# Performance work log

Hardware: AMD Instinct MI355X
Metric: run time of the kernel (lower is better)

The kernel has to match this reference:

```python
import jax, jax.numpy as jnp
import numpy as np
import math

B, S, D, H = 2, 2048, 1024, 16
DK = D // H
NUM_BUCKETS = 32
MAX_DISTANCE = 128


def _relative_position_bucket(relative_position, num_buckets=NUM_BUCKETS, max_distance=MAX_DISTANCE):
    # Bidirectional bucketing, faithful to the torch implementation.
    nb = num_buckets // 2
    n = -relative_position
    ret = (n < 0).astype(jnp.int32) * nb
    n = jnp.abs(n)
    max_exact = nb // 2
    is_small = n < max_exact
    # guard log(0); is_small branch covers n < max_exact anyway
    val_if_large = max_exact + (
        jnp.log(jnp.maximum(n, 1).astype(jnp.float32) / max_exact)
        / math.log(max_distance / max_exact)
        * (nb - max_exact)
    ).astype(jnp.int32)
    val_if_large = jnp.minimum(val_if_large, nb - 1)
    return ret + jnp.where(is_small, n, val_if_large)


def setup_inputs() -> dict:
    key = jax.random.key(0)
    ks = jax.random.split(key, 6)
    scale = 1.0 / math.sqrt(D)
    return {
        "hidden_states": jax.random.normal(ks[0], (B, S, D), dtype=jnp.float32),
        "Wq": jax.random.normal(ks[1], (D, D), dtype=jnp.float32) * scale,
        "Wk": jax.random.normal(ks[2], (D, D), dtype=jnp.float32) * scale,
        "Wv": jax.random.normal(ks[3], (D, D), dtype=jnp.float32) * scale,
        "Wo": jax.random.normal(ks[4], (D, D), dtype=jnp.float32) * scale,
        "rel_emb": jax.random.normal(ks[5], (NUM_BUCKETS, H), dtype=jnp.float32) * 0.1,
    }


def reference(hidden_states, Wq, Wk, Wv, Wo, rel_emb):
    b, s, d = hidden_states.shape
    # nn.Linear convention: y = x @ W.T
    q = jnp.einsum("bsd,ed->bse", hidden_states, Wq).reshape(b, s, H, DK).transpose(0, 2, 1, 3)
    k = jnp.einsum("bsd,ed->bse", hidden_states, Wk).reshape(b, s, H, DK).transpose(0, 2, 1, 3)
    v = jnp.einsum("bsd,ed->bse", hidden_states, Wv).reshape(b, s, H, DK).transpose(0, 2, 1, 3)
    scores = jnp.einsum("bhqd,bhkd->bhqk", q, k) / math.sqrt(DK)  # [B,H,S,S]
    # T5 relative position bias
    ctx = jnp.arange(s)[:, None]
    mem = jnp.arange(s)[None, :]
    rp_bucket = _relative_position_bucket(mem - ctx)          # [S,S]
    bias = rel_emb[rp_bucket]                                  # [S,S,H]
    bias = bias.transpose(2, 0, 1)[None]                       # [1,H,S,S]
    scores = scores + bias
    attn = jax.nn.softmax(scores, axis=-1)
    out = jnp.einsum("bhqk,bhkd->bhqd", attn, v)               # [B,H,S,DK]
    out = out.transpose(0, 2, 1, 3).reshape(b, s, d)
    return jnp.einsum("bsd,ed->bse", out, Wo)
```

## Files before the change

kernel.cpp:

```cpp
#include <hip/hip_runtime.h>
#include <hip/hip_bf16.h>
#include <cstdint>
#include <cstddef>

typedef __bf16 bf16;
typedef __attribute__((ext_vector_type(8))) __bf16 bf16x8;
typedef __attribute__((ext_vector_type(4))) __bf16 bf16x4;
typedef __attribute__((ext_vector_type(4))) float f32x4;
typedef __attribute__((ext_vector_type(4))) short s16x4;

#define B_ 2
#define S_ 2048
#define D_ 1024
#define H_ 16
#define DK_ 64
#define NROWS (B_*S_)
#define NBIAS 4095
#define LDQ 3072
#define LOG2E 1.44269504f

__device__ __forceinline__ void async16(void* lds, const void* g) {
  __builtin_amdgcn_global_load_lds(
      (const __attribute__((address_space(1))) void*)g,
      (__attribute__((address_space(3))) void*)lds, 16, 0, 0);
}

__device__ __forceinline__ f32x4 mfma16(bf16x8 a, bf16x8 b, f32x4 c) {
  return __builtin_amdgcn_mfma_f32_16x16x32_bf16(a, b, c, 0, 0, 0);
}

__device__ __forceinline__ s16x4 bc4(bf16x4 x) {
  union { bf16x4 b; s16x4 s; } u; u.b = x; return u.s;
}

__device__ __forceinline__ f32x4 mfma16k(bf16x4 a, bf16x4 b, f32x4 c) {
  return __builtin_amdgcn_mfma_f32_16x16x16bf16_1k(bc4(a), bc4(b), c, 0, 0, 0);
}

__device__ __forceinline__ float exp2_hw(float x) {
  return __builtin_amdgcn_exp2f(x);
}

__global__ void prep_kernel(const float* __restrict__ X,
                            const float* __restrict__ Wq, const float* __restrict__ Wk,
                            const float* __restrict__ Wv, const float* __restrict__ Wo,
                            const float* __restrict__ rel_emb,
                            bf16* __restrict__ Xb, bf16* __restrict__ oqkv,
                            bf16* __restrict__ oo, float* __restrict__ tab) {
  const int bid = blockIdx.x;
  const int tid = threadIdx.x;
  if (bid < 4096) {
    int i = bid * 256 + tid;
    float4 v = ((const float4*)X)[i];
    bf16x4 o;
    o[0] = (bf16)v.x; o[1] = (bf16)v.y; o[2] = (bf16)v.z; o[3] = (bf16)v.w;
    ((bf16x4*)Xb)[i] = o;
  } else if (bid < 8192) {
    int widx = bid - 4096;
    int y = widx >> 10;
    const float* src = (y == 0) ? Wq : (y == 1) ? Wk : (y == 2) ? Wv : Wo;
    bf16* dst = (y < 3) ? (oqkv + (size_t)y * D_ * D_) : oo;
    int i = (widx & 1023) * 256 + tid;
    float4 v = ((const float4*)src)[i];
    bf16x4 o;
    o[0] = (bf16)v.x; o[1] = (bf16)v.y; o[2] = (bf16)v.z; o[3] = (bf16)v.w;
    ((bf16x4*)dst)[i] = o;
  } else {
    int idx = (bid - 8192) * 256 + tid;
    if (idx >= H_ * NBIAS) return;
    int h = idx / NBIAS;
    int p = idx - h * NBIAS;
    int rel = p - 2047;
    int n = -rel;
    int ret = 0;
    if (n < 0) { ret = 16; n = -n; }
    int bucket;
    if (n < 8) {
      bucket = ret + n;
    } else {
      double v = log((double)n / 8.0) / log(16.0) * 8.0;
      int vi = 8 + (int)v;
      if (vi > 15) vi = 15;
      bucket = ret + vi;
    }
    tab[idx] = rel_emb[bucket * H_ + h] * LOG2E;
  }
}

template<int OUT_BF16, int MF, int VT_EP>
__global__ __launch_bounds__(256, 3)
void gemm_bt(const bf16* __restrict__ A, const bf16* __restrict__ Bw,
             void* __restrict__ C, bf16* __restrict__ VT, int vThr,
             int M, int N, int K, int colThr, float a0, float a1) {
  __shared__ bf16 smem[MF * 32 * 64 + 128 * 64];
  bf16* As = smem;
  bf16* Bs = smem + MF * 32 * 64;
  const int tid = threadIdx.x;
  const int lane = tid & 63;
  const int w = tid >> 6;
  const int wr = w >> 1, wc = w & 1;
  const int l15 = lane & 15, lhi = lane >> 4;
  const int m0 = blockIdx.y * (MF * 32), n0 = blockIdx.x * 128;
  const float alpha = (n0 < colThr) ? a0 : a1;

  f32x4 acc[MF][4] = {};

  const int urow = tid >> 3;
  const int uswz = (tid & 7) ^ (urow & 7);
  const bf16* ga = A  + (size_t)(m0 + urow) * K + uswz * 8;
  const bf16* gb = Bw + (size_t)(n0 + urow) * K + uswz * 8;

  for (int kt = 0; kt < K; kt += 64) {
#pragma unroll
    for (int rnd = 0; rnd < MF; ++rnd)
      async16(As + tid * 8 + rnd * 2048, ga + kt + (size_t)(rnd * 32) * K);
#pragma unroll
    for (int rnd = 0; rnd < 4; ++rnd)
      async16(Bs + tid * 8 + rnd * 2048, gb + kt + (size_t)(rnd * 32) * K);
    __syncthreads();

#pragma unroll
    for (int kc = 0; kc < 2; ++kc) {
      bf16x8 af[MF], bfr[4];
#pragma unroll
      for (int m = 0; m < MF; ++m) {
        int row = wr * (MF * 16) + m * 16 + l15;
        int off = (row * 64 + kc * 32 + lhi * 8) ^ ((row & 7) << 3);
        af[m] = *(const bf16x8*)&As[off];
      }
#pragma unroll
      for (int n = 0; n < 4; ++n) {
        int row = wc * 64 + n * 16 + l15;
        int off = (row * 64 + kc * 32 + lhi * 8) ^ ((row & 7) << 3);
        bfr[n] = *(const bf16x8*)&Bs[off];
      }
      __builtin_amdgcn_s_setprio(1);
#pragma unroll
      for (int m = 0; m < MF; ++m)
#pragma unroll
        for (int n = 0; n < 4; ++n)
          acc[m][n] = mfma16(af[m], bfr[n], acc[m][n]);
      __builtin_amdgcn_s_setprio(0);
    }
    __syncthreads();
  }

  if (VT_EP && n0 >= vThr) {
    bf16* T = smem;
#pragma unroll
    for (int m = 0; m < MF; ++m)
#pragma unroll
      for (int n = 0; n < 4; ++n)
#pragma unroll
        for (int r = 0; r < 4; ++r) {
          int rl = wr * (MF * 16) + m * 16 + lhi * 4 + r;
          int cl = wc * 64 + n * 16 + l15;
          T[cl * 128 + (rl ^ ((cl & 7) << 3))] = (bf16)(acc[m][n][r] * alpha);
        }
    __syncthreads();
    const int bb = m0 >> 11, s0l = m0 & 2047, d0 = n0 - vThr;
    const int dr = tid >> 1, sh = tid & 1;
    bf16* dst = VT + ((size_t)(bb * 1024 + d0 + dr)) * 2048 + s0l + sh * 64;
    const bf16* src = T + dr * 128;
#pragma unroll
    for (int i = 0; i < 8; ++i) {
      int sb = sh * 8 + i;
      *(bf16x8*)(dst + i * 8) = *(const bf16x8*)(src + ((sb ^ (dr & 7)) * 8));
    }
    return;
  }

#pragma unroll
  for (int m = 0; m < MF; ++m)
#pragma unroll
    for (int n = 0; n < 4; ++n)
#pragma unroll
      for (int r = 0; r < 4; ++r) {
        int row = m0 + wr * (MF * 16) + m * 16 + lhi * 4 + r;
        int col = n0 + wc * 64 + n * 16 + l15;
        float v = acc[m][n][r] * alpha;
        if (OUT_BF16) ((bf16*)C)[(size_t)row * N + col] = (bf16)v;
        else          ((float*)C)[(size_t)row * N + col] = v;
      }
}

__global__ __launch_bounds__(256, 4)
void attn_fwd(const bf16* __restrict__ QKV, const bf16* __restrict__ VTg_,
              const float* __restrict__ biasTab, const float* __restrict__ rel_emb,
              bf16* __restrict__ Og) {
  __shared__ bf16 Ks[2][64 * 64];
  __shared__ bf16 VTs[2][64 * 64];
  __shared__ float bias_s[512];
  const int tid = threadIdx.x;
  const int lane = tid & 63, w = tid >> 6;
  const int l15 = lane & 15, lhi = lane >> 4;
  const int wg = blockIdx.x;
  const int bh = wg & 31, qt = wg >> 5;
  const int b = bh >> 4, h = bh & 15;
  const int q0 = qt * 64;

  for (int i = tid; i < 512; i += 256)
    bias_s[i] = biasTab[h * NBIAS + 1791 + i];

  const float cL = rel_emb[15 * H_ + h] * LOG2E;
  const float cR = rel_emb[31 * H_ + h] * LOG2E;

  bf16x8 qa[2];
  {
    const bf16* Qbase = QKV + (size_t)(b * S_ + q0 + w * 16) * LDQ + h * DK_;
#pragma unroll
    for (int c = 0; c < 2; ++c)
      qa[c] = *(const bf16x8*)(Qbase + (size_t)l15 * LDQ + c * 32 + lhi * 8);
  }

  int koff[8];
#pragma unroll
  for (int kf = 0; kf < 4; ++kf)
#pragma unroll
    for (int c = 0; c < 2; ++c) {
      int krow = kf * 16 + l15;
      koff[kf * 2 + c] = ((krow * 64 + c * 32 + lhi * 8) ^ ((krow & 7) << 3)) * 2;
    }
  int voff[16];
#pragma unroll
  for (int df = 0; df < 4; ++df)
#pragma unroll
    for (int kf = 0; kf < 4; ++kf)
      voff[df * 4 + kf] =
          (((df * 16 + l15) * 64 + kf * 16 + lhi * 4) * 2) ^ ((l15 & 7) << 4);

  float lpart = 0.f;
  f32x4 oacc[4] = {};

  const int urow = tid >> 3;
  const int uswz = (tid & 7) ^ (urow & 7);
  const bf16* gk = QKV  + (size_t)(b * S_) * LDQ + 1024 + h * DK_
                        + (size_t)urow * LDQ + uswz * 8;
  const bf16* gv = VTg_ + (size_t)(b * 1024 + h * DK_) * 2048
                        + (size_t)urow * 2048 + uswz * 8;

  async16(&Ks[0][tid * 8],         gk);
  async16(&Ks[0][tid * 8 + 2048],  gk + 32 * LDQ);
  async16(&VTs[0][tid * 8],        gv);
  async16(&VTs[0][tid * 8 + 2048], gv + 32 * 2048);
  gk += 64 * LDQ;
  gv += 64;
  __syncthreads();

#define TILE_BODY(CUR, KT, DO_PF)                                              \
  do {                                                                         \
    if (DO_PF) {                                                               \
      async16(&Ks[(CUR) ^ 1][tid * 8],         gk);                            \
      async16(&Ks[(CUR) ^ 1][tid * 8 + 2048],  gk + 32 * LDQ);                 \
      async16(&VTs[(CUR) ^ 1][tid * 8],        gv);                            \
      async16(&VTs[(CUR) ^ 1][tid * 8 + 2048], gv + 32 * 2048);                \
      gk += 64 * LDQ;                                                          \
      gv += 64;                                                                \
    }                                                                          \
    const int dk0 = (KT) - q0;                                                 \
    f32x4 st[4];                                                               \
    if (dk0 >= -128 && dk0 <= 128) {                                           \
      const int bb0 = dk0 + lhi * 4 - (w * 16 + l15) + 256;                    \
      _Pragma("unroll")                                                        \
      for (int kf = 0; kf < 4; ++kf)                                           \
        _Pragma("unroll")                                                      \
        for (int r = 0; r < 4; ++r)                                            \
          st[kf][r] = bias_s[bb0 + kf * 16 + r];                               \
    } else {                                                                   \
      const float cq = (dk0 > 0) ? cR : cL;                                    \
      _Pragma("unroll")                                                        \
      for (int kf = 0; kf < 4; ++kf)                                           \
        _Pragma("unroll")                                                      \
        for (int r = 0; r < 4; ++r)                                            \
          st[kf][r] = cq;                                                      \
    }                                                                          \
    _Pragma("unroll")                                                          \
    for (int kf = 0; kf < 4; ++kf) {                                           \
      _Pragma("unroll")                                                        \
      for (int c = 0; c < 2; ++c) {                                            \
        bf16x8 kb = *(const bf16x8*)((const char*)&Ks[CUR][0] +                \
                                     koff[kf * 2 + c]);                        \
        st[kf] = mfma16(kb, qa[c], st[kf]);                                    \
      }                                                                        \
    }                                                                          \
    bf16x4 pa[4];                                                              \
    float rs = 0.f;                                                            \
    _Pragma("unroll")                                                          \
    for (int kf = 0; kf < 4; ++kf)                                             \
      _Pragma("unroll")                                                        \
      for (int r = 0; r < 4; ++r) {                                            \
        float p = exp2_hw(st[kf][r]);                                          \
        rs += p;                                                               \
        pa[kf][r] = (bf16)p;                                                   \
      }                                                                        \
    lpart += rs;                                                               \
    _Pragma("unroll")                                                          \
    for (int df = 0; df < 4; ++df) {                                           \
      bf16x4 vb[4];                                                            \
      _Pragma("unroll")                                                        \
      for (int kf = 0; kf < 4; ++kf)                                           \
        vb[kf] = *(const bf16x4*)((const char*)&VTs[CUR][0] +                  \
                                  voff[df * 4 + kf]);                          \
      _Pragma("unroll")                                                        \
      for (int kf = 0; kf < 4; ++kf)                                           \
        oacc[df] = mfma16k(pa[kf], vb[kf], oacc[df]);                          \
    }                                                                          \
    __syncthreads();                                                           \
  } while (0)

  for (int tt = 0; tt < 16; ++tt) {
    const int ktbase = tt * 128;
    TILE_BODY(0, ktbase, true);
    TILE_BODY(1, ktbase + 64, tt < 15);
  }
#undef TILE_BODY

  float lr0 = lpart;
  lr0 += __shfl_xor(lr0, 16);
  lr0 += __shfl_xor(lr0, 32);
#pragma unroll
  for (int r = 0; r < 4; ++r) {
    float lr = __shfl(lr0, lhi * 4 + r);
    float inv = 1.0f / lr;
#pragma unroll
    for (int df = 0; df < 4; ++df) {
      int row = b * S_ + q0 + w * 16 + lhi * 4 + r;
      int col = h * DK_ + df * 16 + l15;
      Og[(size_t)row * D_ + col] = (bf16)(oacc[df][r] * inv);
    }
  }
}

extern "C" void kernel_launch(void* const* d_in, const int* in_sizes, int n_in,
                              void* d_out, int out_size, void* d_ws, size_t ws_size,
                              hipStream_t stream) {
  const float* X   = (const float*)d_in[0];
  const float* Wq  = (const float*)d_in[1];
  const float* Wk  = (const float*)d_in[2];
  const float* Wv  = (const float*)d_in[3];
  const float* Wo  = (const float*)d_in[4];
  const float* rel = (const float*)d_in[5];
  float* out = (float*)d_out;
  char* ws = (char*)d_ws;
  const size_t MB = 1u << 20;
  bf16* Xb    = (bf16*)(ws + 0 * MB);
  bf16* Wqkvb = (bf16*)(ws + 8 * MB);
  bf16* Wob   = (bf16*)(ws + 14 * MB);
  bf16* QKVb  = (bf16*)(ws + 16 * MB);
  bf16* VTb   = (bf16*)(ws + 40 * MB);
  float* biasTab = (float*)(ws + 48 * MB);

  prep_kernel<<<8448, 256, 0, stream>>>(X, Wq, Wk, Wv, Wo, rel,
                                        Xb, Wqkvb, Wob, biasTab);

  gemm_bt<1, 4, 1><<<dim3(24, 32), 256, 0, stream>>>(Xb, Wqkvb, QKVb,
      VTb, 2048,
      NROWS, 3 * D_, D_, 1024, 0.125f * LOG2E, 1.0f);

  attn_fwd<<<1024, 256, 0, stream>>>(QKVb, VTb, biasTab, rel, Xb );

  gemm_bt<0, 2, 0><<<dim3(8, 64), 256, 0, stream>>>(Xb, Wob, out,
      nullptr, 1 << 30,
      NROWS, D_, D_, 0, 1.0f, 1.0f);
}
```

Measured before the change: 114.9 us.

## Process two query fragments per wave to double K/V tile reuse in attention

Each attention workgroup now covers 128 query rows instead of 64, with each wave holding two 16-row Q fragments, so every K and V^T tile loaded into LDS feeds twice as many MFMAs. The grid halves to 512 blocks and launch bounds drop to 2 waves per SIMD to leave room for the doubled accumulators. The bias window indexing is adjusted for the wider query span. The aim is to halve K/V global and LDS traffic per unit of work, at the cost of fewer blocks (fewer than two per CU on 256 CUs) and lower occupancy.

```diff
diff --git a/kernel.cpp b/kernel.cpp
--- a/kernel.cpp
+++ b/kernel.cpp
@@ -184,7 +184,7 @@
       }
 }
 
-__global__ __launch_bounds__(256, 4)
+__global__ __launch_bounds__(256, 2)
 void attn_fwd(const bf16* __restrict__ QKV, const bf16* __restrict__ VTg_,
               const float* __restrict__ biasTab, const float* __restrict__ rel_emb,
               bf16* __restrict__ Og) {
@@ -197,20 +197,22 @@
   const int wg = blockIdx.x;
   const int bh = wg & 31, qt = wg >> 5;
   const int b = bh >> 4, h = bh & 15;
-  const int q0 = qt * 64;
-
-  for (int i = tid; i < 512; i += 256)
-    bias_s[i] = biasTab[h * NBIAS + 1791 + i];
+  const int q0 = qt * 128;
+
+  for (int i = tid; i < 511; i += 256)
+    bias_s[i] = biasTab[h * NBIAS + 1792 + i];
 
   const float cL = rel_emb[15 * H_ + h] * LOG2E;
   const float cR = rel_emb[31 * H_ + h] * LOG2E;
 
-  bf16x8 qa[2];
+  bf16x8 qa[2][2];
   {
-    const bf16* Qbase = QKV + (size_t)(b * S_ + q0 + w * 16) * LDQ + h * DK_;
-#pragma unroll
-    for (int c = 0; c < 2; ++c)
-      qa[c] = *(const bf16x8*)(Qbase + (size_t)l15 * LDQ + c * 32 + lhi * 8);
+    const bf16* Qbase = QKV + (size_t)(b * S_ + q0 + w * 32) * LDQ + h * DK_;
+#pragma unroll
+    for (int qf = 0; qf < 2; ++qf)
+#pragma unroll
+      for (int c = 0; c < 2; ++c)
+        qa[qf][c] = *(const bf16x8*)(Qbase + (size_t)(qf * 16 + l15) * LDQ + c * 32 + lhi * 8);
   }
 
   int koff[8];
@@ -229,8 +231,8 @@
       voff[df * 4 + kf] =
           (((df * 16 + l15) * 64 + kf * 16 + lhi * 4) * 2) ^ ((l15 & 7) << 4);
 
-  float lpart = 0.f;
-  f32x4 oacc[4] = {};
+  float lpart[2] = {0.f, 0.f};
+  f32x4 oacc[2][4] = {};
 
   const int urow = tid >> 3;
   const int uswz = (tid & 7) ^ (urow & 7);
@@ -258,21 +260,25 @@
       gv += 64;                                                                \
     }                                                                          \
     const int dk0 = (KT) - q0;                                                 \
-    f32x4 st[4];                                                               \
-    if (dk0 >= -128 && dk0 <= 128) {                                           \
-      const int bb0 = dk0 + lhi * 4 - (w * 16 + l15) + 256;                    \
-      _Pragma("unroll")                                                        \
-      for (int kf = 0; kf < 4; ++kf)                                           \
+    f32x4 st[2][4];                                                            \
+    if (dk0 >= -128 && dk0 <= 192) {                                           \
+      const int bb0 = dk0 + lhi * 4 - w * 32 - l15 + 255;                      \
+      _Pragma("unroll")                                                        \
+      for (int qf = 0; qf < 2; ++qf)                                           \
         _Pragma("unroll")                                                      \
-        for (int r = 0; r < 4; ++r)                                            \
-          st[kf][r] = bias_s[bb0 + kf * 16 + r];                               \
+        for (int kf = 0; kf < 4; ++kf)                                         \
+          _Pragma("unroll")                                                    \
+          for (int r = 0; r < 4; ++r)                                          \
+            st[qf][kf][r] = bias_s[bb0 + (kf - qf) * 16 + r];                  \
     } else {                                                                   \
       const float cq = (dk0 > 0) ? cR : cL;                                    \
       _Pragma("unroll")                                                        \
-      for (int kf = 0; kf < 4; ++kf)                                           \
+      for (int qf = 0; qf < 2; ++qf)                                           \
         _Pragma("unroll")                                                      \
-        for (int r = 0; r < 4; ++r)                                            \
-          st[kf][r] = cq;                                                      \
+        for (int kf = 0; kf < 4; ++kf)                                         \
+          _Pragma("unroll")                                                    \
+          for (int r = 0; r < 4; ++r)                                          \
+            st[qf][kf][r] = cq;                                                \
     }                                                                          \
     _Pragma("unroll")                                                          \
     for (int kf = 0; kf < 4; ++kf) {                                           \
@@ -280,20 +286,24 @@
       for (int c = 0; c < 2; ++c) {                                            \
         bf16x8 kb = *(const bf16x8*)((const char*)&Ks[CUR][0] +                \
                                      koff[kf * 2 + c]);                        \
-        st[kf] = mfma16(kb, qa[c], st[kf]);                                    \
+        st[0][kf] = mfma16(kb, qa[0][c], st[0][kf]);                           \
+        st[1][kf] = mfma16(kb, qa[1][c], st[1][kf]);                           \
       }                                                                        \
     }                                                                          \
-    bf16x4 pa[4];                                                              \
-    float rs = 0.f;                                                            \
+    bf16x4 pa[2][4];                                                           \
     _Pragma("unroll")                                                          \
-    for (int kf = 0; kf < 4; ++kf)                                             \
-      _Pragma("unroll")                                                        \
-      for (int r = 0; r < 4; ++r) {                                            \
-        float p = exp2_hw(st[kf][r]);                                          \
-        rs += p;                                                               \
-        pa[kf][r] = (bf16)p;                                                   \
-      }                                                                        \
-    lpart += rs;                                                               \
+    for (int qf = 0; qf < 2; ++qf) {                                           \
+      float rs = 0.f;                                                          \
+      _Pragma("unroll")                                                        \
+      for (int kf = 0; kf < 4; ++kf)                                           \
+        _Pragma("unroll")                                                      \
+        for (int r = 0; r < 4; ++r) {                                          \
+          float p = exp2_hw(st[qf][kf][r]);                                    \
+          rs += p;                                                             \
+          pa[qf][kf][r] = (bf16)p;                                             \
+        }                                                                      \
+      lpart[qf] += rs;                                                         \
+    }                                                                          \
     _Pragma("unroll")                                                          \
     for (int df = 0; df < 4; ++df) {                                           \
       bf16x4 vb[4];                                                            \
@@ -302,8 +312,10 @@
         vb[kf] = *(const bf16x4*)((const char*)&VTs[CUR][0] +                  \
                                   voff[df * 4 + kf]);                          \
       _Pragma("unroll")                                                        \
-      for (int kf = 0; kf < 4; ++kf)                                           \
-        oacc[df] = mfma16k(pa[kf], vb[kf], oacc[df]);                          \
+      for (int qf = 0; qf < 2; ++qf)                                           \
+        _Pragma("unroll")                                                      \
+        for (int kf = 0; kf < 4; ++kf)                                         \
+          oacc[qf][df] = mfma16k(pa[qf][kf], vb[kf], oacc[qf][df]);            \
     }                                                                          \
     __syncthreads();                                                           \
   } while (0)
@@ -315,18 +327,21 @@
   }
 #undef TILE_BODY
 
-  float lr0 = lpart;
-  lr0 += __shfl_xor(lr0, 16);
-  lr0 += __shfl_xor(lr0, 32);
-#pragma unroll
-  for (int r = 0; r < 4; ++r) {
-    float lr = __shfl(lr0, lhi * 4 + r);
-    float inv = 1.0f / lr;
-#pragma unroll
-    for (int df = 0; df < 4; ++df) {
-      int row = b * S_ + q0 + w * 16 + lhi * 4 + r;
-      int col = h * DK_ + df * 16 + l15;
-      Og[(size_t)row * D_ + col] = (bf16)(oacc[df][r] * inv);
+#pragma unroll
+  for (int qf = 0; qf < 2; ++qf) {
+    float lr0 = lpart[qf];
+    lr0 += __shfl_xor(lr0, 16);
+    lr0 += __shfl_xor(lr0, 32);
+#pragma unroll
+    for (int r = 0; r < 4; ++r) {
+      float lr = __shfl(lr0, lhi * 4 + r);
+      float inv = 1.0f / lr;
+#pragma unroll
+      for (int df = 0; df < 4; ++df) {
+        int row = b * S_ + q0 + w * 32 + qf * 16 + lhi * 4 + r;
+        int col = h * DK_ + df * 16 + l15;
+        Og[(size_t)row * D_ + col] = (bf16)(oacc[qf][df][r] * inv);
+      }
     }
   }
 }
@@ -357,7 +372,7 @@
       VTb, 2048,
       NROWS, 3 * D_, D_, 1024, 0.125f * LOG2E, 1.0f);
 
-  attn_fwd<<<1024, 256, 0, stream>>>(QKVb, VTb, biasTab, rel, Xb );
+  attn_fwd<<<512, 256, 0, stream>>>(QKVb, VTb, biasTab, rel, Xb );
 
   gemm_bt<0, 2, 0><<<dim3(8, 64), 256, 0, stream>>>(Xb, Wob, out,
       nullptr, 1 << 30,
```

After: 111.7 us. 2.8% less time.
